# Performance work log

Hardware: AMD Instinct MI355X
Metric: run time of the kernel (lower is better)

The kernel has to match this reference:

```python
import jax, jax.numpy as jnp
import numpy as np

B, N, D = 512, 101, 128
H = D
NHEADS = 8
HD = H // NHEADS
NSTEPS = 140


def setup_inputs() -> dict:
    key = jax.random.key(0)
    ks = jax.random.split(key, 12)
    enc = jax.random.normal(ks[0], (B, N, D), jnp.float32)
    pool = jax.random.normal(ks[1], (B, H), jnp.float32)
    # CVRP-style demands: depot demand 0, customers in (0, 0.2); capacity normalized to 1.0
    demand = jax.random.uniform(ks[2], (B, N), jnp.float32) * 0.2
    demand = demand.at[:, 0].set(0.0)
    capcity = jnp.ones((B, 1), jnp.float32)
    actions_old = jax.random.randint(ks[3], (B, NSTEPS), 0, N, dtype=jnp.int32)

    def lin(k, fin, fout):
        return (jax.random.normal(k, (fin, fout), jnp.float32) / np.sqrt(fin)).astype(jnp.float32)

    return dict(
        encoder_inputs=enc, pool=pool, actions_old=actions_old,
        capcity=capcity, demand=demand, n_steps=NSTEPS, batch_size=B,
        W_fc=lin(ks[4], H + 1, H),      # Decoder1.fc  (no bias)
        W_fc1=lin(ks[5], H, H),         # Decoder1.fc1
        W_w=lin(ks[6], D, H),           # Attention1.w (cat=1)
        W_k=lin(ks[7], D, H),           # Attention1.k
        W_v=lin(ks[8], D, H),           # Attention1.v
        W_attnfc=lin(ks[9], H, H),      # Attention1.fc
        W_pk=lin(ks[10], D, H),         # ProbAttention.k
    )


def reference(encoder_inputs, pool, actions_old, capcity, demand, n_steps, batch_size,
              W_fc, W_fc1, W_w, W_k, W_v, W_attnfc, W_pk):
    Bs, Nn, Dd = encoder_inputs.shape
    Hh = W_fc.shape[1]
    nh = NHEADS
    hd = Hh // nh
    cap0 = capcity[0, 0]  # torch: capcity[0].item()
    demands = demand
    col = jnp.arange(Nn)

    # context is constant across decode steps -> hoist K/V/pointer-K projections
    Kh = (encoder_inputs @ W_k).reshape(Bs, Nn, nh, hd).transpose(0, 2, 1, 3)  # (B,h,N,hd)
    Vh = (encoder_inputs @ W_v).reshape(Bs, Nn, nh, hd).transpose(0, 2, 1, 3)
    Kp = encoder_inputs @ W_pk  # (B,N,H)

    def update_mask(mask1, dyn_cap, index):
        # mask1: visited nodes (bool). depot masked iff we just arrived at depot.
        go_depot = index == 0
        m1 = jnp.logical_or(mask1, col[None, :] == index[:, None])
        m1 = m1.at[:, 0].set(go_depot)
        mask = jnp.logical_or(m1, demands > dyn_cap)  # dyn_cap (B,1) broadcasts
        # guard: if everything masked (instance finished), allow depot (torch code
        # breaks out of the loop instead; log_p is zeroed by is_done either way)
        all_masked = jnp.all(mask, axis=1)
        mask = mask.at[:, 0].set(jnp.where(all_masked, False, mask[:, 0]))
        return mask, m1

    def update_state(dyn_cap, index):
        cur = jnp.take_along_axis(demands, index[:, None], axis=1)
        dyn = dyn_cap - cur
        return jnp.where((index == 0)[:, None], cap0, dyn)

    mask1_init = jnp.zeros((Bs, Nn), bool)
    idx0 = jnp.zeros((Bs,), jnp.int32)
    mask_init, mask1_init = update_mask(mask1_init, capcity, idx0)  # i == 0 update

    def step(carry, _):
        _input, dyn_cap, mask, mask1, pool_c = carry
        dec = jnp.concatenate([_input, dyn_cap], axis=-1) @ W_fc  # (B,H)
        pool_n = pool_c @ W_fc1                                   # pool re-projected EVERY step (as in torch)
        dec = dec + pool_n
        # --- Attention1 (multi-head glimpse) ---
        Q = (dec @ W_w).reshape(Bs, nh, hd)
        compat = jnp.einsum('bhd,bhnd->bhn', Q, Kh) * (1.0 / np.sqrt(hd))
        u = jnp.where(mask[:, None, :], -jnp.inf, compat)
        sc = jax.nn.softmax(u, axis=-1)
        glimpse = jnp.einsum('bhn,bhnd->bhd', sc, Vh).reshape(Bs, Hh) @ W_attnfc
        # --- ProbAttention (tanh-clipped pointer) ---
        comp2 = jnp.einsum('bh,bnh->bn', glimpse, Kp) * (1.0 / np.sqrt(Hh))
        logits = jnp.where(mask, -jnp.inf, 10.0 * jnp.tanh(comp2))
        logp_all = jax.nn.log_softmax(logits, axis=-1)
        index = jnp.argmax(logp_all, axis=-1)  # greedy decode
        log_p = jnp.take_along_axis(logp_all, index[:, None], axis=1)[:, 0]
        is_done = (jnp.sum(mask1[:, 1:].astype(jnp.int32), axis=1) >= (Nn - 1)).astype(log_p.dtype)
        log_p = log_p * (1.0 - is_done)
        dyn_new = jax.lax.stop_gradient(update_state(dyn_cap, index))  # torch .detach()
        mask_new, mask1_new = update_mask(mask1, dyn_new, index)
        inp_new = jnp.take_along_axis(encoder_inputs, index[:, None, None], axis=1)[:, 0, :]
        return (inp_new, dyn_new, mask_new, mask1_new, pool_n), (index, log_p)

    carry0 = (encoder_inputs[:, 0, :], capcity, mask_init, mask1_init, pool)
    _, (actions, log_ps) = jax.lax.scan(step, carry0, None, length=int(n_steps))
    actions = actions.T            # (B, n_steps)
    log_p = jnp.sum(log_ps, axis=0)  # (B,)
    return actions, log_p
```

## Files before the change

### kernel.cpp

```cpp
#include <hip/hip_runtime.h>
#include <math.h>

#define B_ 512
#define N_ 101
#define H_ 128
#define T_ 140
#define M37 0x1FFFFFFFFFull

#define BAR() asm volatile("s_waitcnt lgkmcnt(0)\n\ts_barrier" ::: "memory")
#define LGKM0() asm volatile("s_waitcnt lgkmcnt(0)" ::: "memory")

template <int CTRL, int RM>
__device__ __forceinline__ float dpp_max_step(float x) {
  int t = __builtin_amdgcn_update_dpp((int)0xFF800000, __float_as_int(x), CTRL, RM, 0xF, false);
  return fmaxf(x, __int_as_float(t));
}
template <int CTRL, int RM>
__device__ __forceinline__ float dpp_add_step(float x) {
  int t = __builtin_amdgcn_update_dpp(0, __float_as_int(x), CTRL, RM, 0xF, false);
  return x + __int_as_float(t);
}
__device__ __forceinline__ float wave_max64(float x) {
  x = dpp_max_step<0x111, 0xF>(x);
  x = dpp_max_step<0x112, 0xF>(x);
  x = dpp_max_step<0x114, 0xF>(x);
  x = dpp_max_step<0x118, 0xF>(x);
  x = dpp_max_step<0x142, 0xA>(x);
  x = dpp_max_step<0x143, 0xC>(x);
  return __int_as_float(__builtin_amdgcn_readlane(__float_as_int(x), 63));
}
__device__ __forceinline__ float wave_sum64(float x) {
  x = dpp_add_step<0x111, 0xF>(x);
  x = dpp_add_step<0x112, 0xF>(x);
  x = dpp_add_step<0x114, 0xF>(x);
  x = dpp_add_step<0x118, 0xF>(x);
  x = dpp_add_step<0x142, 0xA>(x);
  x = dpp_add_step<0x143, 0xC>(x);
  return __int_as_float(__builtin_amdgcn_readlane(__float_as_int(x), 63));
}

__device__ __forceinline__ float bfly_xor16(float x) {
  return __int_as_float(__builtin_amdgcn_ds_swizzle(__float_as_int(x), 0x401F));
}
__device__ __forceinline__ float bfly_xor8(float x) {
  int xi = __float_as_int(x);
  int t = __builtin_amdgcn_update_dpp(xi, xi, 0x128, 0xF, 0xF, false);
  return __int_as_float(t);
}
__device__ __forceinline__ float bfly_xor4(float x) {
  int xi = __float_as_int(x);
  int t = __builtin_amdgcn_update_dpp(xi, xi, 0x104, 0xF, 0x5, false);
  t = __builtin_amdgcn_update_dpp(t, xi, 0x114, 0xF, 0xA, false);
  return __int_as_float(t);
}
__device__ __forceinline__ float bfly_xor2(float x) {
  int xi = __float_as_int(x);
  int t = __builtin_amdgcn_update_dpp(xi, xi, 0x4E, 0xF, 0xF, false);
  return __int_as_float(t);
}
__device__ __forceinline__ float bfly_xor1(float x) {
  int xi = __float_as_int(x);
  int t = __builtin_amdgcn_update_dpp(xi, xi, 0xB1, 0xF, 0xF, false);
  return __int_as_float(t);
}

__device__ __forceinline__ void gemm_tile_dev(
    const float* A, const float* B, float* C, int cb, int transB, int tid)
{
  int cc = cb * 32 + (tid & 7) * 4;
  int r0 = tid >> 3;
  float4 acc0 = {0,0,0,0}, acc1 = {0,0,0,0}, acc2 = {0,0,0,0}, acc3 = {0,0,0,0};
  for (int k4 = 0; k4 < 32; ++k4) {
    const int k = k4 * 4;
    float4 a0v = *(const float4*)(A + (r0 +  0) * 128 + k);
    float4 a1v = *(const float4*)(A + (r0 + 32) * 128 + k);
    float4 a2v = *(const float4*)(A + (r0 + 64) * 128 + k);
    float4 a3v = *(const float4*)(A + (r0 + 96) * 128 + k);
    float4 b0, b1, b2, b3;
    if (!transB) {
      b0 = *(const float4*)(B + (k + 0) * 128 + cc);
      b1 = *(const float4*)(B + (k + 1) * 128 + cc);
      b2 = *(const float4*)(B + (k + 2) * 128 + cc);
      b3 = *(const float4*)(B + (k + 3) * 128 + cc);
    } else {
      float4 t0 = *(const float4*)(B + (cc + 0) * 128 + k);
      float4 t1 = *(const float4*)(B + (cc + 1) * 128 + k);
      float4 t2 = *(const float4*)(B + (cc + 2) * 128 + k);
      float4 t3 = *(const float4*)(B + (cc + 3) * 128 + k);
      b0 = make_float4(t0.x, t1.x, t2.x, t3.x);
      b1 = make_float4(t0.y, t1.y, t2.y, t3.y);
      b2 = make_float4(t0.z, t1.z, t2.z, t3.z);
      b3 = make_float4(t0.w, t1.w, t2.w, t3.w);
    }
#define GSTEP(AC, BV) \
    acc0.x += a0v.AC * BV.x; acc0.y += a0v.AC * BV.y; acc0.z += a0v.AC * BV.z; acc0.w += a0v.AC * BV.w; \
    acc1.x += a1v.AC * BV.x; acc1.y += a1v.AC * BV.y; acc1.z += a1v.AC * BV.z; acc1.w += a1v.AC * BV.w; \
    acc2.x += a2v.AC * BV.x; acc2.y += a2v.AC * BV.y; acc2.z += a2v.AC * BV.z; acc2.w += a2v.AC * BV.w; \
    acc3.x += a3v.AC * BV.x; acc3.y += a3v.AC * BV.y; acc3.z += a3v.AC * BV.z; acc3.w += a3v.AC * BV.w;
    GSTEP(x, b0)
    GSTEP(y, b1)
    GSTEP(z, b2)
    GSTEP(w, b3)
#undef GSTEP
  }
  *(float4*)(C + (r0 +  0) * 128 + cc) = acc0;
  *(float4*)(C + (r0 + 32) * 128 + cc) = acc1;
  *(float4*)(C + (r0 + 64) * 128 + cc) = acc2;
  *(float4*)(C + (r0 + 96) * 128 + cc) = acc3;
}

__global__ __launch_bounds__(256) void stage_a(
    const float* __restrict__ Wfc, const float* __restrict__ Ww,
    const float* __restrict__ Wpk, const float* __restrict__ Wat,
    const float* __restrict__ F,
    float* __restrict__ Wfw, float* __restrict__ Wc, float* __restrict__ wcap,
    float* __restrict__ Mbuf)
{
  int j = blockIdx.x, tid = threadIdx.x;
  if (j < 4)       gemm_tile_dev(Wfc, Ww, Wfw, j, 0, tid);
  else if (j < 8)  gemm_tile_dev(Wpk, Wat, Wc, j - 4, 1, tid);
  else if (j == 8) {
    if (tid < 128) {
      float s = 0.f;
      for (int k = 0; k < 128; ++k) s += Wfc[128 * 128 + k] * Ww[k * 128 + tid];
      wcap[tid] = s;
    }
  } else gemm_tile_dev(F, F, Mbuf + 2ll * 16384, j - 9, 0, tid);
}

__global__ __launch_bounds__(256) void stage_b(
    const float* __restrict__ F, const float* __restrict__ enc,
    const float* __restrict__ Wfw, float* __restrict__ Mbuf,
    float* __restrict__ encW)
{
  int bx = blockIdx.x, tid = threadIdx.x;
  if (bx < 8) {
    int s = (bx >> 2) + 1, cb = bx & 3;
    const float* As = (s == 1) ? F : Mbuf + (long long)s * 16384;
    gemm_tile_dev(As, Mbuf + 2ll * 16384, Mbuf + (long long)(2 + s) * 16384, cb, 0, tid);
  } else {
    int jj = bx - 8, rb = jj >> 2, cb = jj & 3;
    gemm_tile_dev(enc + (long long)rb * 16384, Wfw, encW + (long long)rb * 16384, cb, 0, tid);
  }
}

__global__ __launch_bounds__(256) void chainL(
    const float* __restrict__ F, float* __restrict__ Mbuf, int L)
{
  int bx = blockIdx.x, tid = threadIdx.x;
  int s = (bx >> 2) + 1, cb = bx & 3;
  const float* As = (s == 1) ? F : Mbuf + (long long)s * 16384;
  gemm_tile_dev(As, Mbuf + (long long)L * 16384, Mbuf + (long long)(L + s) * 16384, cb, 0, tid);
}

__global__ __launch_bounds__(256) void stage_n8(
    const float* __restrict__ F, const float* __restrict__ Ww,
    float* __restrict__ Mbuf, float* __restrict__ Abuf)
{
  int bx = blockIdx.x, tid = threadIdx.x;
  if (bx < 48) {
    int s = (bx >> 2) + 1, cb = bx & 3;
    const float* As = (s == 1) ? F : Mbuf + (long long)s * 16384;
    gemm_tile_dev(As, Mbuf + 128ll * 16384, Mbuf + (long long)(128 + s) * 16384, cb, 0, tid);
  } else {
    int jj = bx - 48, t = jj >> 2, cb = jj & 3;
    const float* Ms = (t == 0) ? F : Mbuf + (long long)(t + 1) * 16384;
    gemm_tile_dev(Ms, Ww, Abuf + (long long)t * 16384, cb, 0, tid);
  }
}

__global__ __launch_bounds__(256) void stage_n9(
    const float* __restrict__ Ww, const float* __restrict__ pool,
    float* __restrict__ Mbuf, float* __restrict__ Abuf, float* __restrict__ Qpl)
{
  int bx = blockIdx.x, tid = threadIdx.x;
  if (bx < 52) {
    int t = 127 + (bx >> 2), cb = bx & 3;
    gemm_tile_dev(Mbuf + (long long)(t + 1) * 16384, Ww, Abuf + (long long)t * 16384, cb, 0, tid);
  } else {
    int jj = bx - 52, t = jj >> 4, sub = jj & 15, rb = sub >> 2, cb = sub & 3;
    gemm_tile_dev(pool + (long long)rb * 16384, Abuf + (long long)t * 16384,
                  Qpl + (long long)t * 65536 + (long long)rb * 16384, cb, 0, tid);
  }
}

__global__ __launch_bounds__(256) void stage_n10(
    const float* __restrict__ pool, float* __restrict__ Abuf, float* __restrict__ Qpl)
{
  int bx = blockIdx.x, tid = threadIdx.x;
  int t = 127 + (bx >> 4), sub = bx & 15, rb = sub >> 2, cb = sub & 3;
  gemm_tile_dev(pool + (long long)rb * 16384, Abuf + (long long)t * 16384,
                Qpl + (long long)t * 65536 + (long long)rb * 16384, cb, 0, tid);
}

__device__ __forceinline__ void compat_sm(
    int wave, int lane, int amaxU, float capU,
    unsigned long long msklo, unsigned long long mskhi,
    const float* s_buf, const float* s_wc, const float* s_qp,
    float* s_qs, const float* kreg, float* s_sc)
{
  if (lane < 32) {
    int d = (lane < 16) ? (wave * 16 + lane) : ((wave + 4) * 16 + (lane - 16));
    float qv = s_buf[amaxU * H_ + d] + capU * s_wc[d] + s_qp[d];
    s_qs[wave * 32 + lane] = qv;
  }
  LGKM0();
  const float4* q0 = (const float4*)(s_qs + wave * 32);
  const float4* q1 = (const float4*)(s_qs + wave * 32 + 16);
  float c00 = 0.f, c01 = 0.f, c10 = 0.f, c11 = 0.f;
#pragma unroll
  for (int q = 0; q < 4; ++q) {
    float4 qq = q0[q];
    c00 += qq.x * kreg[q * 4 + 0] + qq.y * kreg[q * 4 + 1]
         + qq.z * kreg[q * 4 + 2] + qq.w * kreg[q * 4 + 3];
    c10 += qq.x * kreg[32 + q * 4 + 0] + qq.y * kreg[32 + q * 4 + 1]
         + qq.z * kreg[32 + q * 4 + 2] + qq.w * kreg[32 + q * 4 + 3];
    float4 qr = q1[q];
    c01 += qr.x * kreg[16 + q * 4 + 0] + qr.y * kreg[16 + q * 4 + 1]
         + qr.z * kreg[16 + q * 4 + 2] + qr.w * kreg[16 + q * 4 + 3];
    c11 += qr.x * kreg[48 + q * 4 + 0] + qr.y * kreg[48 + q * 4 + 1]
         + qr.z * kreg[48 + q * 4 + 2] + qr.w * kreg[48 + q * 4 + 3];
  }
  bool mb0 = (msklo >> lane) & 1ull;
  bool mb1v = (lane < 37) ? ((mskhi >> lane) & 1ull) : true;
  float a0 = mb0 ? -INFINITY : 0.25f * c00;
  float a1 = mb0 ? -INFINITY : 0.25f * c01;
  float b0 = mb1v ? -INFINITY : 0.25f * c10;
  float b1 = mb1v ? -INFINITY : 0.25f * c11;

  float m0  = wave_max64(fmaxf(a0, b0));
  float m1v = wave_max64(fmaxf(a1, b1));
  float ea0 = expf(a0 - m0),  eb0 = (lane < 37) ? expf(b0 - m0)  : 0.f;
  float ea1 = expf(a1 - m1v), eb1 = (lane < 37) ? expf(b1 - m1v) : 0.f;
  float s0 = ea0 + eb0, s1 = ea1 + eb1;
  { float t0 = __shfl_xor(s0, 32), t1 = __shfl_xor(s1, 32); s0 += t0; s1 += t1; }
  { float t0 = bfly_xor16(s0),     t1 = bfly_xor16(s1);     s0 += t0; s1 += t1; }
  { float t0 = bfly_xor8(s0),      t1 = bfly_xor8(s1);      s0 += t0; s1 += t1; }
  { float t0 = bfly_xor4(s0),      t1 = bfly_xor4(s1);      s0 += t0; s1 += t1; }
  { float t0 = bfly_xor2(s0),      t1 = bfly_xor2(s1);      s0 += t0; s1 += t1; }
  { float t0 = bfly_xor1(s0),      t1 = bfly_xor1(s1);      s0 += t0; s1 += t1; }
  float* r0 = s_sc + wave * 104;
  float* r1 = s_sc + (wave + 4) * 104;
  r0[lane] = ea0 / s0; r1[lane] = ea1 / s1;
  if (lane < 37) { r0[64 + lane] = eb0 / s0; r1[64 + lane] = eb1 / s1; }
}

__global__ __attribute__((amdgpu_flat_work_group_size(256, 256), amdgpu_waves_per_eu(2, 2)))
void decode_kernel(
    const float* __restrict__ enc,
    const float* __restrict__ Wk,
    const float* __restrict__ Wv,
    const float* __restrict__ Wc,
    const float* __restrict__ encW,
    const float* __restrict__ Qpool,
    const float* __restrict__ wcap,
    const float* __restrict__ capcity,
    const float* __restrict__ demand,
    float* __restrict__ out)
{
  __shared__ __align__(16) float s_buf[N_ * 132];
  __shared__ __align__(16) float s_sc[8 * 104];
  __shared__ __align__(16) float s_part[128];
  __shared__ __align__(16) float s_p2[256];
  __shared__ __align__(16) float s_qs[128];
  __shared__ __align__(16) float s_wc[128];
  __shared__ __align__(16) float s_qp[128];

  const int b    = blockIdx.x;
  const int tid  = threadIdx.x;
  const int lane = tid & 63;
  const int wave = tid >> 6;
  const int an = tid & 127, aj = tid >> 7;
  const int bh2 = (lane >> 4) & 1;
  const int bj2 = (wave + ((lane >= 32) ? 4 : 0)) * 16 + (lane & 15);
  const float invSqrtH = 0.08838834764831845f;

  float cap  = capcity[b];
  float cap0 = capcity[0];
  float dem0 = demand[(long long)b * N_ + lane];
  float dem1 = (lane < 37) ? demand[(long long)b * N_ + 64 + lane] : 0.f;
  float wcr  = (tid < 128) ? wcap[tid] : 0.f;
  float qp0  = (tid < 128) ? Qpool[(long long)b * H_ + tid] : 0.f;

  for (int idx = tid; idx < N_ * 32; idx += 256) {
    int row = idx >> 5, q = idx & 31;
    float4 v = *(const float4*)(enc + ((long long)b * N_ + row) * H_ + q * 4);
    float* d = s_buf + row * 132 + q * 4;
    d[0] = v.x; d[1] = v.y; d[2] = v.z; d[3] = v.w;
  }
  BAR();

  float vreg[51];
#pragma unroll
  for (int q = 0; q < 51; ++q) vreg[q] = 0.f;
  {
    const int base = bh2 * 51;
    for (int i4 = 0; i4 < 32; ++i4) {
      float w0 = Wv[(i4 * 4 + 0) * H_ + bj2];
      float w1 = Wv[(i4 * 4 + 1) * H_ + bj2];
      float w2 = Wv[(i4 * 4 + 2) * H_ + bj2];
      float w3 = Wv[(i4 * 4 + 3) * H_ + bj2];
#pragma unroll
      for (int nl = 0; nl < 51; ++nl) {
        if (base + nl < N_) {
          float4 e = *(const float4*)(s_buf + (base + nl) * 132 + i4 * 4);
          vreg[nl] += e.x * w0 + e.y * w1 + e.z * w2 + e.w * w3;
        }
      }
    }
  }

  float kreg[64];
#pragma unroll
  for (int q = 0; q < 64; ++q) kreg[q] = 0.f;
  {
    const int n0 = lane;
    const int n1c = (lane < 37) ? 64 + lane : 0;
    for (int i = 0; i < 128; ++i) {
      float e0 = s_buf[n0 * 132 + i];
      float e1 = s_buf[n1c * 132 + i];
      const float4* wk0 = (const float4*)(Wk + i * H_ + wave * 16);
      const float4* wk1 = (const float4*)(Wk + i * H_ + (wave + 4) * 16);
#pragma unroll
      for (int q = 0; q < 4; ++q) {
        float4 a = wk0[q];
        kreg[q * 4 + 0] += e0 * a.x; kreg[q * 4 + 1] += e0 * a.y;
        kreg[q * 4 + 2] += e0 * a.z; kreg[q * 4 + 3] += e0 * a.w;
        kreg[32 + q * 4 + 0] += e1 * a.x; kreg[32 + q * 4 + 1] += e1 * a.y;
        kreg[32 + q * 4 + 2] += e1 * a.z; kreg[32 + q * 4 + 3] += e1 * a.w;
        float4 c = wk1[q];
        kreg[16 + q * 4 + 0] += e0 * c.x; kreg[16 + q * 4 + 1] += e0 * c.y;
        kreg[16 + q * 4 + 2] += e0 * c.z; kreg[16 + q * 4 + 3] += e0 * c.w;
        kreg[48 + q * 4 + 0] += e1 * c.x; kreg[48 + q * 4 + 1] += e1 * c.y;
        kreg[48 + q * 4 + 2] += e1 * c.z; kreg[48 + q * 4 + 3] += e1 * c.w;
      }
    }
  }

  float preg[64];
#pragma unroll
  for (int q = 0; q < 64; ++q) preg[q] = 0.f;
  if (an < N_) {
    for (int i = 0; i < 128; ++i) {
      float e = s_buf[an * 132 + i];
      const float4* wc = (const float4*)(Wc + i * H_ + aj * 64);
#pragma unroll
      for (int q = 0; q < 16; ++q) {
        float4 c = wc[q];
        preg[q * 4 + 0] += e * c.x; preg[q * 4 + 1] += e * c.y;
        preg[q * 4 + 2] += e * c.z; preg[q * 4 + 3] += e * c.w;
      }
    }
  }
  BAR();

  for (int idx = tid; idx < N_ * 32; idx += 256) {
    int row = idx >> 5, q = idx & 31;
    float4 v = *(const float4*)(encW + ((long long)b * N_ + row) * H_ + q * 4);
    float* d = s_buf + row * 128 + q * 4;
    d[0] = v.x; d[1] = v.y; d[2] = v.z; d[3] = v.w;
  }
  if (tid < 128) { s_wc[tid] = wcr; s_qp[tid] = qp0; }
  BAR();

  unsigned long long m1lo = 1ull, m1hi = 0ull;
  unsigned long long msklo, mskhi;
  {
    bool p0i = (lane == 0) || (dem0 > cap);
    bool p1i = (lane < 37) ? (dem1 > cap) : true;
    msklo = __ballot(p0i);
    mskhi = __ballot(p1i) & M37;
    if (msklo == ~0ull && mskhi == M37) msklo &= ~1ull;
  }
  float logpAcc = 0.f;
  compat_sm(wave, lane, 0, cap, msklo, mskhi, s_buf, s_wc, s_qp, s_qs, kreg, s_sc);

  for (int t = 0; t < T_; ++t) {
    int tn = (t + 1 < T_) ? (t + 1) : t;
    float qn = (tid < 128) ? Qpool[((long long)tn * B_ + b) * H_ + tid] : 0.f;

    {
      LGKM0();
      const float* srow = s_sc + (bj2 >> 4) * 104;
      float acc = 0.f;
      if (bh2 == 0) {
#pragma unroll
        for (int q = 0; q < 12; ++q) {
          float4 sv = *(const float4*)(srow + q * 4);
          acc += sv.x * vreg[q * 4 + 0] + sv.y * vreg[q * 4 + 1]
               + sv.z * vreg[q * 4 + 2] + sv.w * vreg[q * 4 + 3];
        }
        acc += srow[48] * vreg[48] + srow[49] * vreg[49] + srow[50] * vreg[50];
      } else {
        acc += srow[51] * vreg[0];
#pragma unroll
        for (int q = 0; q < 12; ++q) {
          float4 sv = *(const float4*)(srow + 52 + q * 4);
          acc += sv.x * vreg[1 + q * 4] + sv.y * vreg[2 + q * 4]
               + sv.z * vreg[3 + q * 4] + sv.w * vreg[4 + q * 4];
        }
        acc += srow[100] * vreg[49];
      }
      float gl = acc + bfly_xor16(acc);
      if (bh2 == 0) s_part[bj2] = gl;
    }
    BAR();

    if (an < N_) {
      const float4* p0 = (const float4*)(s_part + aj * 64);
      float c = 0.f;
#pragma unroll
      for (int q = 0; q < 16; ++q) {
        float4 g0 = p0[q];
        c += g0.x * preg[q * 4 + 0] + g0.y * preg[q * 4 + 1]
           + g0.z * preg[q * 4 + 2] + g0.w * preg[q * 4 + 3];
      }
      s_p2[aj * 128 + an] = c;
    }
    if (tid < 128) s_qp[tid] = qn;
    BAR();

    {
      float l0 = -INFINITY, l1 = -INFINITY;
      bool mb0 = (msklo >> lane) & 1ull;
      if (!mb0) l0 = 10.f * tanhf((s_p2[lane] + s_p2[128 + lane]) * invSqrtH);
      if (lane < 37) {
        bool mb1 = (mskhi >> lane) & 1ull;
        if (!mb1) l1 = 10.f * tanhf((s_p2[64 + lane] + s_p2[192 + lane]) * invSqrtH);
      }
      float vmax = wave_max64(fmaxf(l0, l1));
      unsigned long long blo = __ballot(l0 == vmax);
      unsigned long long bhi = __ballot(l1 == vmax);
      int amax = blo ? (__ffsll((long long)blo) - 1)
                     : (64 + __ffsll((long long)bhi) - 1);
      if (wave == 0) {
        float ss = wave_sum64(__expf(l0 - vmax) + __expf(l1 - vmax));
        logpAcc -= __logf(ss);
      }

      float dlo = __int_as_float(__builtin_amdgcn_readlane(__float_as_int(dem0), amax & 63));
      float dhi = __int_as_float(__builtin_amdgcn_readlane(__float_as_int(dem1), amax & 63));
      float capNew = (amax == 0) ? cap0 : (cap - ((amax < 64) ? dlo : dhi));
      if (amax < 64) m1lo |= (1ull << amax); else m1hi |= (1ull << (amax - 64));
      m1lo = (m1lo & ~1ull) | (unsigned long long)(amax == 0);
      bool doneNew = ((int)__popcll(m1lo & ~1ull) + (int)__popcll(m1hi)) >= (N_ - 1);
      bool p0m = ((m1lo >> lane) & 1ull) || (dem0 > capNew);
      bool p1m = (lane < 37) ? (((m1hi >> lane) & 1ull) || (dem1 > capNew)) : true;
      unsigned long long klo = __ballot(p0m);
      unsigned long long khi = __ballot(p1m) & M37;
      if (klo == ~0ull && khi == M37) klo &= ~1ull;
      msklo = klo; mskhi = khi; cap = capNew;

      if (tid == 0) out[(long long)b * T_ + t] = (float)amax;
      if (doneNew) {
        for (int tt = t + 1 + tid; tt < T_; tt += 256)
          out[(long long)b * T_ + tt] = 0.f;
        break;
      }
      if (t + 1 < T_)
        compat_sm(wave, lane, amax, capNew, msklo, mskhi,
                  s_buf, s_wc, s_qp, s_qs, kreg, s_sc);
    }
  }

  if (tid == 0) out[(long long)B_ * T_ + b] = logpAcc;
}

extern "C" void kernel_launch(void* const* d_in, const int* in_sizes, int n_in,
                              void* d_out, int out_size, void* d_ws, size_t ws_size,
                              hipStream_t stream)
{
  const float* enc   = (const float*)d_in[0];
  const float* pool  = (const float*)d_in[1];
  const float* cap   = (const float*)d_in[3];
  const float* dem   = (const float*)d_in[4];
  const float* W_fc  = (const float*)d_in[7];
  const float* W_fc1 = (const float*)d_in[8];
  const float* W_w   = (const float*)d_in[9];
  const float* W_kk  = (const float*)d_in[10];
  const float* W_vv  = (const float*)d_in[11];
  const float* W_at  = (const float*)d_in[12];
  const float* W_pk  = (const float*)d_in[13];
  float* out = (float*)d_out;
  float* ws  = (float*)d_ws;

  float* Mbuf  = ws;
  float* Abuf  = Mbuf + 141 * 16384;
  float* Qpl   = Abuf + 140 * 16384;
  float* encW  = Qpl + 140 * 512 * 128;
  float* Wfw   = encW + 512 * 101 * 128;
  float* Wc    = Wfw + 16384;
  float* wcapb = Wc + 16384;

  stage_a<<<13, 256, 0, stream>>>(W_fc, W_w, W_pk, W_at, W_fc1, Wfw, Wc, wcapb, Mbuf);
  stage_b<<<1624, 256, 0, stream>>>(W_fc1, enc, Wfw, Mbuf, encW);
  chainL<<<16, 256, 0, stream>>>(W_fc1, Mbuf, 4);
  chainL<<<32, 256, 0, stream>>>(W_fc1, Mbuf, 8);
  chainL<<<64, 256, 0, stream>>>(W_fc1, Mbuf, 16);
  chainL<<<128, 256, 0, stream>>>(W_fc1, Mbuf, 32);
  chainL<<<256, 256, 0, stream>>>(W_fc1, Mbuf, 64);
  stage_n8<<<556, 256, 0, stream>>>(W_fc1, W_w, Mbuf, Abuf);
  stage_n9<<<2084, 256, 0, stream>>>(W_w, pool, Mbuf, Abuf, Qpl);
  stage_n10<<<208, 256, 0, stream>>>(pool, Abuf, Qpl);
  decode_kernel<<<512, 256, 0, stream>>>(enc, W_kk, W_vv, Wc, encW, Qpl, wcapb, cap, dem, out);
}
```

Baseline: 983.6 us.

## Merge matrix-power chain launches into one cooperative kernel with grid syncs

Replaces the five chainL launches and the chain part of stage_n8 with a single cooperative kernel that runs the doubling chain of W_fc1 powers, separated by grid-wide syncs. The A-projection and Qp GEMMs, which were previously interleaved across stage_n8/n9/n10 to overlap with the chain tail, now run as two plain launches after the chain finishes. The goal is to cut kernel launch gaps in the dependent prologue. In exchange it loses the overlap of the last chain stages with the projection work and adds grid-sync costs.

```diff
diff --git a/kernel.cpp b/kernel.cpp
--- a/kernel.cpp
+++ b/kernel.cpp
@@ -1,5 +1,8 @@
 #include <hip/hip_runtime.h>
+#include <hip/hip_cooperative_groups.h>
 #include <math.h>
+
+namespace cg = cooperative_groups;
 
 #define B_ 512
 #define N_ 101
@@ -144,51 +147,63 @@
   }
 }
 
-__global__ __launch_bounds__(256) void chainL(
-    const float* __restrict__ F, float* __restrict__ Mbuf, int L)
-{
+__global__ __launch_bounds__(256) void chain_coop(
+    const float* __restrict__ F, float* __restrict__ Mbuf)
+{
+  cg::grid_group grid = cg::this_grid();
   int bx = blockIdx.x, tid = threadIdx.x;
-  int s = (bx >> 2) + 1, cb = bx & 3;
-  const float* As = (s == 1) ? F : Mbuf + (long long)s * 16384;
-  gemm_tile_dev(As, Mbuf + (long long)L * 16384, Mbuf + (long long)(L + s) * 16384, cb, 0, tid);
-}
-
-__global__ __launch_bounds__(256) void stage_n8(
+  if (bx < 16) {
+    int s = (bx >> 2) + 1, cb = bx & 3;
+    const float* As = (s == 1) ? F : Mbuf + (long long)s * 16384;
+    gemm_tile_dev(As, Mbuf + 4ll * 16384, Mbuf + (long long)(4 + s) * 16384, cb, 0, tid);
+  }
+  grid.sync();
+  if (bx < 32) {
+    int s = (bx >> 2) + 1, cb = bx & 3;
+    const float* As = (s == 1) ? F : Mbuf + (long long)s * 16384;
+    gemm_tile_dev(As, Mbuf + 8ll * 16384, Mbuf + (long long)(8 + s) * 16384, cb, 0, tid);
+  }
+  grid.sync();
+  if (bx < 64) {
+    int s = (bx >> 2) + 1, cb = bx & 3;
+    const float* As = (s == 1) ? F : Mbuf + (long long)s * 16384;
+    gemm_tile_dev(As, Mbuf + 16ll * 16384, Mbuf + (long long)(16 + s) * 16384, cb, 0, tid);
+  }
+  grid.sync();
+  if (bx < 128) {
+    int s = (bx >> 2) + 1, cb = bx & 3;
+    const float* As = (s == 1) ? F : Mbuf + (long long)s * 16384;
+    gemm_tile_dev(As, Mbuf + 32ll * 16384, Mbuf + (long long)(32 + s) * 16384, cb, 0, tid);
+  }
+  grid.sync();
+  {
+    int s = (bx >> 2) + 1, cb = bx & 3;
+    const float* As = (s == 1) ? F : Mbuf + (long long)s * 16384;
+    gemm_tile_dev(As, Mbuf + 64ll * 16384, Mbuf + (long long)(64 + s) * 16384, cb, 0, tid);
+  }
+  grid.sync();
+  if (bx < 48) {
+    int s = (bx >> 2) + 1, cb = bx & 3;
+    const float* As = (s == 1) ? F : Mbuf + (long long)s * 16384;
+    gemm_tile_dev(As, Mbuf + 128ll * 16384, Mbuf + (long long)(128 + s) * 16384, cb, 0, tid);
+  }
+}
+
+__global__ __launch_bounds__(256) void stage_At(
     const float* __restrict__ F, const float* __restrict__ Ww,
     float* __restrict__ Mbuf, float* __restrict__ Abuf)
 {
   int bx = blockIdx.x, tid = threadIdx.x;
-  if (bx < 48) {
-    int s = (bx >> 2) + 1, cb = bx & 3;
-    const float* As = (s == 1) ? F : Mbuf + (long long)s * 16384;
-    gemm_tile_dev(As, Mbuf + 128ll * 16384, Mbuf + (long long)(128 + s) * 16384, cb, 0, tid);
-  } else {
-    int jj = bx - 48, t = jj >> 2, cb = jj & 3;
-    const float* Ms = (t == 0) ? F : Mbuf + (long long)(t + 1) * 16384;
-    gemm_tile_dev(Ms, Ww, Abuf + (long long)t * 16384, cb, 0, tid);
-  }
-}
-
-__global__ __launch_bounds__(256) void stage_n9(
-    const float* __restrict__ Ww, const float* __restrict__ pool,
-    float* __restrict__ Mbuf, float* __restrict__ Abuf, float* __restrict__ Qpl)
+  int t = bx >> 2, cb = bx & 3;
+  const float* Ms = (t == 0) ? F : Mbuf + (long long)(t + 1) * 16384;
+  gemm_tile_dev(Ms, Ww, Abuf + (long long)t * 16384, cb, 0, tid);
+}
+
+__global__ __launch_bounds__(256) void stage_Qp(
+    const float* __restrict__ pool, float* __restrict__ Abuf, float* __restrict__ Qpl)
 {
   int bx = blockIdx.x, tid = threadIdx.x;
-  if (bx < 52) {
-    int t = 127 + (bx >> 2), cb = bx & 3;
-    gemm_tile_dev(Mbuf + (long long)(t + 1) * 16384, Ww, Abuf + (long long)t * 16384, cb, 0, tid);
-  } else {
-    int jj = bx - 52, t = jj >> 4, sub = jj & 15, rb = sub >> 2, cb = sub & 3;
-    gemm_tile_dev(pool + (long long)rb * 16384, Abuf + (long long)t * 16384,
-                  Qpl + (long long)t * 65536 + (long long)rb * 16384, cb, 0, tid);
-  }
-}
-
-__global__ __launch_bounds__(256) void stage_n10(
-    const float* __restrict__ pool, float* __restrict__ Abuf, float* __restrict__ Qpl)
-{
-  int bx = blockIdx.x, tid = threadIdx.x;
-  int t = 127 + (bx >> 4), sub = bx & 15, rb = sub >> 2, cb = sub & 3;
+  int t = bx >> 4, sub = bx & 15, rb = sub >> 2, cb = sub & 3;
   gemm_tile_dev(pool + (long long)rb * 16384, Abuf + (long long)t * 16384,
                 Qpl + (long long)t * 65536 + (long long)rb * 16384, cb, 0, tid);
 }
@@ -494,13 +509,14 @@
 
   stage_a<<<13, 256, 0, stream>>>(W_fc, W_w, W_pk, W_at, W_fc1, Wfw, Wc, wcapb, Mbuf);
   stage_b<<<1624, 256, 0, stream>>>(W_fc1, enc, Wfw, Mbuf, encW);
-  chainL<<<16, 256, 0, stream>>>(W_fc1, Mbuf, 4);
-  chainL<<<32, 256, 0, stream>>>(W_fc1, Mbuf, 8);
-  chainL<<<64, 256, 0, stream>>>(W_fc1, Mbuf, 16);
-  chainL<<<128, 256, 0, stream>>>(W_fc1, Mbuf, 32);
-  chainL<<<256, 256, 0, stream>>>(W_fc1, Mbuf, 64);
-  stage_n8<<<556, 256, 0, stream>>>(W_fc1, W_w, Mbuf, Abuf);
-  stage_n9<<<2084, 256, 0, stream>>>(W_w, pool, Mbuf, Abuf, Qpl);
-  stage_n10<<<208, 256, 0, stream>>>(pool, Abuf, Qpl);
+
+  {
+    void* cargs[] = { (void*)&W_fc1, (void*)&Mbuf };
+    hipLaunchCooperativeKernel((const void*)chain_coop, dim3(256), dim3(256),
+                               cargs, 0, stream);
+  }
+
+  stage_At<<<560, 256, 0, stream>>>(W_fc1, W_w, Mbuf, Abuf);
+  stage_Qp<<<2240, 256, 0, stream>>>(pool, Abuf, Qpl);
   decode_kernel<<<512, 256, 0, stream>>>(enc, W_kk, W_vv, Wc, encW, Qpl, wcapb, cap, dem, out);
 }
```

New measurement: 1.098 ms. +11.6%, slower.

## Merge precompute GEMM stages into a pipelined generic kernel with interleaved work

Applied to the files above, without the earlier changes.

Replaces the separate stage_b, chainL, n8, n9 and n10 kernels with a single parameterized stage_pipe kernel. Each launch mixes the next matrix-power doubling step with A-projection, pool-projection and encoder-projection tiles whose inputs are already ready. The small serial chain launches get filled with independent work and the whole pipeline stays at a similar launch count. This depends on the hand-computed block counts and offsets staying consistent with the data dependencies, and an error there would silently read stale buffers.

```diff
diff --git a/kernel.cpp b/kernel.cpp
--- a/kernel.cpp
+++ b/kernel.cpp
@@ -128,69 +128,34 @@
   } else gemm_tile_dev(F, F, Mbuf + 2ll * 16384, j - 9, 0, tid);
 }
 
-__global__ __launch_bounds__(256) void stage_b(
-    const float* __restrict__ F, const float* __restrict__ enc,
-    const float* __restrict__ Wfw, float* __restrict__ Mbuf,
-    float* __restrict__ encW)
+__global__ __launch_bounds__(256) void stage_pipe(
+    const float* __restrict__ F, const float* __restrict__ Ww,
+    const float* __restrict__ pool, const float* __restrict__ enc,
+    const float* __restrict__ Wfw,
+    float* __restrict__ Mbuf, float* __restrict__ Abuf,
+    float* __restrict__ Qpl, float* __restrict__ encW,
+    int L, int nc, int a0, int na, int q0, int nq, int e0)
 {
   int bx = blockIdx.x, tid = threadIdx.x;
-  if (bx < 8) {
+  int c_end = 4 * nc, a_end = c_end + 4 * na, q_end = a_end + 16 * nq;
+  if (bx < c_end) {
     int s = (bx >> 2) + 1, cb = bx & 3;
     const float* As = (s == 1) ? F : Mbuf + (long long)s * 16384;
-    gemm_tile_dev(As, Mbuf + 2ll * 16384, Mbuf + (long long)(2 + s) * 16384, cb, 0, tid);
-  } else {
-    int jj = bx - 8, rb = jj >> 2, cb = jj & 3;
-    gemm_tile_dev(enc + (long long)rb * 16384, Wfw, encW + (long long)rb * 16384, cb, 0, tid);
-  }
-}
-
-__global__ __launch_bounds__(256) void chainL(
-    const float* __restrict__ F, float* __restrict__ Mbuf, int L)
-{
-  int bx = blockIdx.x, tid = threadIdx.x;
-  int s = (bx >> 2) + 1, cb = bx & 3;
-  const float* As = (s == 1) ? F : Mbuf + (long long)s * 16384;
-  gemm_tile_dev(As, Mbuf + (long long)L * 16384, Mbuf + (long long)(L + s) * 16384, cb, 0, tid);
-}
-
-__global__ __launch_bounds__(256) void stage_n8(
-    const float* __restrict__ F, const float* __restrict__ Ww,
-    float* __restrict__ Mbuf, float* __restrict__ Abuf)
-{
-  int bx = blockIdx.x, tid = threadIdx.x;
-  if (bx < 48) {
-    int s = (bx >> 2) + 1, cb = bx & 3;
-    const float* As = (s == 1) ? F : Mbuf + (long long)s * 16384;
-    gemm_tile_dev(As, Mbuf + 128ll * 16384, Mbuf + (long long)(128 + s) * 16384, cb, 0, tid);
-  } else {
-    int jj = bx - 48, t = jj >> 2, cb = jj & 3;
+    gemm_tile_dev(As, Mbuf + (long long)L * 16384,
+                  Mbuf + (long long)(L + s) * 16384, cb, 0, tid);
+  } else if (bx < a_end) {
+    int j = bx - c_end, t = a0 + (j >> 2), cb = j & 3;
     const float* Ms = (t == 0) ? F : Mbuf + (long long)(t + 1) * 16384;
     gemm_tile_dev(Ms, Ww, Abuf + (long long)t * 16384, cb, 0, tid);
-  }
-}
-
-__global__ __launch_bounds__(256) void stage_n9(
-    const float* __restrict__ Ww, const float* __restrict__ pool,
-    float* __restrict__ Mbuf, float* __restrict__ Abuf, float* __restrict__ Qpl)
-{
-  int bx = blockIdx.x, tid = threadIdx.x;
-  if (bx < 52) {
-    int t = 127 + (bx >> 2), cb = bx & 3;
-    gemm_tile_dev(Mbuf + (long long)(t + 1) * 16384, Ww, Abuf + (long long)t * 16384, cb, 0, tid);
-  } else {
-    int jj = bx - 52, t = jj >> 4, sub = jj & 15, rb = sub >> 2, cb = sub & 3;
+  } else if (bx < q_end) {
+    int j = bx - a_end, t = q0 + (j >> 4), sub = j & 15, rb = sub >> 2, cb = sub & 3;
     gemm_tile_dev(pool + (long long)rb * 16384, Abuf + (long long)t * 16384,
                   Qpl + (long long)t * 65536 + (long long)rb * 16384, cb, 0, tid);
-  }
-}
-
-__global__ __launch_bounds__(256) void stage_n10(
-    const float* __restrict__ pool, float* __restrict__ Abuf, float* __restrict__ Qpl)
-{
-  int bx = blockIdx.x, tid = threadIdx.x;
-  int t = 127 + (bx >> 4), sub = bx & 15, rb = sub >> 2, cb = sub & 3;
-  gemm_tile_dev(pool + (long long)rb * 16384, Abuf + (long long)t * 16384,
-                Qpl + (long long)t * 65536 + (long long)rb * 16384, cb, 0, tid);
+  } else {
+    int j = e0 + (bx - q_end), rb = j >> 2, cb = j & 3;
+    gemm_tile_dev(enc + (long long)rb * 16384, Wfw,
+                  encW + (long long)rb * 16384, cb, 0, tid);
+  }
 }
 
 __device__ __forceinline__ void compat_sm(
@@ -493,14 +458,25 @@
   float* wcapb = Wc + 16384;
 
   stage_a<<<13, 256, 0, stream>>>(W_fc, W_w, W_pk, W_at, W_fc1, Wfw, Wc, wcapb, Mbuf);
-  stage_b<<<1624, 256, 0, stream>>>(W_fc1, enc, Wfw, Mbuf, encW);
-  chainL<<<16, 256, 0, stream>>>(W_fc1, Mbuf, 4);
-  chainL<<<32, 256, 0, stream>>>(W_fc1, Mbuf, 8);
-  chainL<<<64, 256, 0, stream>>>(W_fc1, Mbuf, 16);
-  chainL<<<128, 256, 0, stream>>>(W_fc1, Mbuf, 32);
-  chainL<<<256, 256, 0, stream>>>(W_fc1, Mbuf, 64);
-  stage_n8<<<556, 256, 0, stream>>>(W_fc1, W_w, Mbuf, Abuf);
-  stage_n9<<<2084, 256, 0, stream>>>(W_w, pool, Mbuf, Abuf, Qpl);
-  stage_n10<<<208, 256, 0, stream>>>(pool, Abuf, Qpl);
+
+  stage_pipe<<<512, 256, 0, stream>>>(W_fc1, W_w, pool, enc, Wfw, Mbuf, Abuf, Qpl, encW,
+                                      2, 2,   0, 0,   0, 0,   0);
+  stage_pipe<<<512, 256, 0, stream>>>(W_fc1, W_w, pool, enc, Wfw, Mbuf, Abuf, Qpl, encW,
+                                      4, 4,   0, 4,   0, 0,   504);
+  stage_pipe<<<512, 256, 0, stream>>>(W_fc1, W_w, pool, enc, Wfw, Mbuf, Abuf, Qpl, encW,
+                                      8, 8,   4, 4,   0, 4,   984);
+  stage_pipe<<<392, 256, 0, stream>>>(W_fc1, W_w, pool, enc, Wfw, Mbuf, Abuf, Qpl, encW,
+                                      16, 16, 8, 8,   4, 4,   1384);
+  stage_pipe<<<320, 256, 0, stream>>>(W_fc1, W_w, pool, enc, Wfw, Mbuf, Abuf, Qpl, encW,
+                                      32, 32, 16, 16, 8, 8,   0);
+  stage_pipe<<<640, 256, 0, stream>>>(W_fc1, W_w, pool, enc, Wfw, Mbuf, Abuf, Qpl, encW,
+                                      64, 64, 32, 32, 16, 16, 0);
+  stage_pipe<<<816, 256, 0, stream>>>(W_fc1, W_w, pool, enc, Wfw, Mbuf, Abuf, Qpl, encW,
+                                      128, 12, 64, 64, 32, 32, 0);
+  stage_pipe<<<1072, 256, 0, stream>>>(W_fc1, W_w, pool, enc, Wfw, Mbuf, Abuf, Qpl, encW,
+                                      0, 0,   128, 12, 64, 64, 0);
+  stage_pipe<<<192, 256, 0, stream>>>(W_fc1, W_w, pool, enc, Wfw, Mbuf, Abuf, Qpl, encW,
+                                      0, 0,   0, 0,   128, 12, 0);
+
   decode_kernel<<<512, 256, 0, stream>>>(enc, W_kk, W_vv, Wc, encW, Qpl, wcapb, cap, dem, out);
 }
```

New measurement: 940.7 us. 1.05x faster.
